# Performance work log

Hardware: AMD Instinct MI355X
Metric: run time of the kernel (lower is better)

## Reference

```python
import jax, jax.numpy as jnp
import numpy as np

L, H, NH, FF = 12, 768, 12, 3072
HD = H // NH
B, T = 8, 512
SCALE = 1.0 / float(np.sqrt(HD))
EPS = 1e-12


def setup_inputs() -> dict:
    key = jax.random.key(0)
    ks = jax.random.split(key, 10)
    s = jnp.float32(0.02)

    def p(k, shape):
        return jax.random.normal(k, shape, dtype=jnp.float32) * s

    return {
        "hidden_states": jax.random.normal(ks[0], (B, T, H), dtype=jnp.float32),
        "attention_mask": jnp.ones((B, T), dtype=jnp.float32),
        "Wq": p(ks[1], (L, H, H)), "bq": jnp.zeros((L, H), jnp.float32),
        "Wk": p(ks[2], (L, H, H)), "bk": jnp.zeros((L, H), jnp.float32),
        "Wv": p(ks[3], (L, H, H)), "bv": jnp.zeros((L, H), jnp.float32),
        "Wao": p(ks[4], (L, H, H)), "bao": jnp.zeros((L, H), jnp.float32),
        "ln1_g": jnp.ones((L, H), jnp.float32), "ln1_b": jnp.zeros((L, H), jnp.float32),
        "Wi": p(ks[5], (L, H, FF)), "bi": jnp.zeros((L, FF), jnp.float32),
        "Wo": p(ks[6], (L, FF, H)), "bo": jnp.zeros((L, H), jnp.float32),
        "ln2_g": jnp.ones((L, H), jnp.float32), "ln2_b": jnp.zeros((L, H), jnp.float32),
    }


def _layernorm(x, g, b):
    m = jnp.mean(x, axis=-1, keepdims=True)
    v = jnp.mean((x - m) ** 2, axis=-1, keepdims=True)
    return (x - m) * jax.lax.rsqrt(v + EPS) * g + b


def _encoder(hidden_states, attention_mask, params):
    # additive mask: (1 - mask) * -10000, broadcast to [B, 1, 1, T]
    add_mask = (1.0 - attention_mask)[:, None, None, :] * -10000.0

    def layer(x, p):
        wq, bq, wk, bk, wv, bv, wao, bao, g1, b1, wi, bi, wo, bo, g2, b2 = p
        q = (x @ wq + bq).reshape(B, T, NH, HD)
        k = (x @ wk + bk).reshape(B, T, NH, HD)
        v = (x @ wv + bv).reshape(B, T, NH, HD)
        scores = jnp.einsum('bihd,bjhd->bhij', q, k) * SCALE + add_mask
        probs = jax.nn.softmax(scores, axis=-1)  # dropout p=0 (eval)
        ctx = jnp.einsum('bhij,bjhd->bihd', probs, v).reshape(B, T, H)
        attn_out = _layernorm(ctx @ wao + bao + x, g1, b1)
        ff = jax.nn.gelu(attn_out @ wi + bi, approximate=False)
        out = _layernorm(ff @ wo + bo + attn_out, g2, b2)
        return out, None

    out, _ = jax.lax.scan(layer, hidden_states, params)
    return out


def reference(hidden_states, attention_mask, Wq, bq, Wk, bk, Wv, bv, Wao, bao,
              ln1_g, ln1_b, Wi, bi, Wo, bo, ln2_g, ln2_b):
    params = (Wq, bq, Wk, bk, Wv, bv, Wao, bao, ln1_g, ln1_b, Wi, bi, Wo, bo, ln2_g, ln2_b)
    return _encoder(hidden_states, attention_mask, params)
```

## Files before the change

kernel.cpp:

```cpp
#include <hip/hip_runtime.h>
#include <hip/hip_bf16.h>

typedef __bf16 bf16;
typedef __attribute__((ext_vector_type(8))) __bf16 bf16x8;
typedef __attribute__((ext_vector_type(4))) float f32x4;

#define MFMA16(a, b, c) __builtin_amdgcn_mfma_f32_16x16x32_bf16((a), (b), (c), 0, 0, 0)

#define WAIT_VM(N) asm volatile("s_waitcnt vmcnt(" #N ")" ::: "memory")
#define BAR() do { __builtin_amdgcn_s_barrier(); __builtin_amdgcn_sched_barrier(0); } while (0)
#define SYNC_VM(N) do { WAIT_VM(N); BAR(); } while (0)
#define SYNC_LGKM() do { asm volatile("s_waitcnt lgkmcnt(0)" ::: "memory"); BAR(); } while (0)

__device__ __forceinline__ void async16(const bf16* g, bf16* l) {
    __builtin_amdgcn_global_load_lds((__attribute__((address_space(1))) void*)(g),
                                     (__attribute__((address_space(3))) void*)(l), 16, 0, 0);
}

__device__ __forceinline__ void xcd_swizzle2(int& bx, int& by) {
    const int gx = gridDim.x, gy = gridDim.y;
    const int nwg = gx * gy;
    const int lin = blockIdx.x + gx * blockIdx.y;
    const int xcd = lin & 7, seq = lin >> 3;
    const int q = nwg >> 3, r = nwg & 7;
    const int nl = (xcd < r ? xcd * (q + 1) : r * (q + 1) + (xcd - r) * q) + seq;
    bx = nl % gx;
    by = nl / gx;
}
__device__ __forceinline__ void xcd_swizzle3(int& bx, int& by, int& bz) {
    const int gx = gridDim.x, gy = gridDim.y;
    const int nwg = gx * gy * gridDim.z;
    const int lin = blockIdx.x + gx * (blockIdx.y + gy * blockIdx.z);
    const int xcd = lin & 7, seq = lin >> 3;
    const int q = nwg >> 3, r = nwg & 7;
    const int nl = (xcd < r ? xcd * (q + 1) : r * (q + 1) + (xcd - r) * q) + seq;
    bx = nl % gx;
    const int t = nl / gx;
    by = t % gy;
    bz = t / gy;
}

__device__ __forceinline__ void xpose_tile(
    int id, const float* Wq, const float* Wk, const float* Wv, const float* Wao,
    const float* Wi, const float* Wo, bf16* wT, bf16* tile, int tid)
{
    const float* src; bf16* dst; int Nd;
    if (id < 576) {
        const int w = id / 144; id -= w * 144;
        Nd = 768;
        src = (w == 0) ? Wq : (w == 1) ? Wk : (w == 2) ? Wv : Wao;
        dst = wT + (size_t)w * 589824;
    } else if (id < 1152) {
        id -= 576; Nd = 3072; src = Wi; dst = wT + 2359296;
    } else {
        id -= 1152; Nd = 768; src = Wo; dst = wT + 4718592;
    }
    const int Kd = (Nd == 3072) ? 768 : ((src == Wo) ? 3072 : 768);
    const int tn = Nd >> 6;
    const int tr = id / tn, tc = id - tr * tn;
    const int r0 = tr * 64, c0 = tc * 64;

#pragma unroll
    for (int i = 0; i < 4; i++) {
        const int idx = i * 256 + tid;
        const int r = idx >> 4, c4 = (idx & 15) * 4;
        const float4 f = *(const float4*)(src + (size_t)(r0 + r) * Nd + c0 + c4);
        alignas(8) bf16 q[4] = {(bf16)f.x, (bf16)f.y, (bf16)f.z, (bf16)f.w};
        *(ushort4*)(tile + r * 68 + c4) = *(ushort4*)q;
    }
    __syncthreads();
#pragma unroll
    for (int i = 0; i < 4; i++) {
        const int idx = i * 256 + tid;
        const int n = idx >> 4, kc = (idx & 15) * 4;
        alignas(8) bf16 tmp[4];
#pragma unroll
        for (int e = 0; e < 4; e++) tmp[e] = tile[(kc + e) * 68 + n];
        *(ushort4*)(dst + (size_t)(c0 + n) * Kd + r0 + kc) = *(ushort4*)tmp;
    }
}

template <int MODE, int BM, int PACK>
__global__ __launch_bounds__(256) void gemm_kernel(
    const bf16* __restrict__ A, const bf16* __restrict__ WT,
    const float* __restrict__ b0, const float* __restrict__ b1, const float* __restrict__ b2,
    int s1, int s2,
    void* __restrict__ o0, void* __restrict__ o1, bf16* __restrict__ vTout,
    const float* __restrict__ xWq, const float* __restrict__ xWk,
    const float* __restrict__ xWv, const float* __restrict__ xWao,
    bf16* __restrict__ wTnext,
    int N, int K, int Kpart)
{
    constexpr int MT = BM / 32;
    constexpr int SBYTES = (2 * (BM * 32) + 2 * (128 * 32)) * 2;
    __shared__ __align__(16) char smem[SBYTES];
    bf16* sA = (bf16*)smem;
    bf16* sB = (bf16*)(smem + 2 * BM * 32 * 2);

    const int tid = threadIdx.x;

    if (PACK && blockIdx.z == 1) {
        const int flat = blockIdx.y * gridDim.x + blockIdx.x;
        if (flat < 576 && wTnext)
            xpose_tile(flat, xWq, xWk, xWv, xWao, nullptr, nullptr, wTnext,
                       (bf16*)smem, tid);
        return;
    }
    const int kslice = PACK ? 0 : blockIdx.z;

    const int lane = tid & 63;
    const int wave = tid >> 6;
    const int quad = lane >> 4;
    const int l15  = lane & 15;
    const int wm   = (wave >> 1) * (BM / 2);
    const int wn   = (wave & 1) * 64;

    int bxs, bys;
    xcd_swizzle2(bxs, bys);
    const int bm = bys * BM;
    const int bn = bxs * 128;
    const int kbase = kslice * Kpart;

    f32x4 acc[MT][4];
#pragma unroll
    for (int i = 0; i < MT; i++)
#pragma unroll
        for (int j = 0; j < 4; j++)
#pragma unroll
            for (int r = 0; r < 4; r++) acc[i][j][r] = 0.0f;

    const int idx1 = tid + 256;
    const int ra0 = tid >> 2,  ca0 = (((tid  & 3) ^ ((ra0 >> 1) & 3)) * 8);
    const int rb1 = idx1 >> 2, cb1 = (((idx1 & 3) ^ ((rb1 >> 1) & 3)) * 8);

    const bf16* Arow0 = A + (size_t)(bm + ra0) * K + kbase + ca0;
    const bf16* Arow1 = (BM == 128) ? A + (size_t)(bm + rb1) * K + kbase + cb1 : A;
    const bf16* Brow0 = WT + (size_t)(bn + ra0) * K + kbase + ca0;
    const bf16* Brow1 = WT + (size_t)(bn + rb1) * K + kbase + cb1;

    const int nk = Kpart >> 5;

    async16(Arow0, sA + tid * 8);
    if (BM == 128) async16(Arow1, sA + idx1 * 8);
    async16(Brow0, sB + tid * 8);
    async16(Brow1, sB + idx1 * 8);

    const int chF = (quad ^ ((l15 >> 1) & 3)) * 8;

    int cur = 0;
    for (int kt = 0; kt < nk; kt++) {
        if (kt + 1 < nk) {
            const int ko = (kt + 1) * 32;
            const int nb = (cur ^ 1);
            async16(Arow0 + ko, sA + nb * BM * 32 + tid * 8);
            if (BM == 128) async16(Arow1 + ko, sA + nb * BM * 32 + idx1 * 8);
            async16(Brow0 + ko, sB + nb * 128 * 32 + tid * 8);
            async16(Brow1 + ko, sB + nb * 128 * 32 + idx1 * 8);
            if (BM == 128) SYNC_VM(4);
            else           SYNC_VM(3);
        } else {
            SYNC_VM(0);
        }
        const bf16* sAc = sA + cur * BM * 32;
        const bf16* sBc = sB + cur * 128 * 32;
        bf16x8 af[MT], bfr[4];
#pragma unroll
        for (int i = 0; i < MT; i++)
            af[i] = *(const bf16x8*)(sAc + (wm + i * 16 + l15) * 32 + chF);
#pragma unroll
        for (int i = 0; i < 4; i++)
            bfr[i] = *(const bf16x8*)(sBc + (wn + i * 16 + l15) * 32 + chF);
#pragma unroll
        for (int mt = 0; mt < MT; mt++)
#pragma unroll
            for (int nt = 0; nt < 4; nt++)
                acc[mt][nt] = MFMA16(af[mt], bfr[nt], acc[mt][nt]);
        SYNC_LGKM();
        cur ^= 1;
    }

    void* outp = (kslice == 0) ? o0 : o1;

#pragma unroll
    for (int nt = 0; nt < 4; nt++) {
        const int col = bn + wn + nt * 16 + l15;
        float bias = 0.0f;
        if (MODE != 1)
            bias = (col < s1) ? b0[col] : (col < s2) ? b1[col - s1] : b2[col - s2];
        if (MODE == 0 && col >= s2) {
            const int hd = col - s2, h = hd >> 6, d = hd & 63;
#pragma unroll
            for (int mt = 0; mt < MT; mt++) {
                const int row0 = bm + wm + mt * 16 + quad * 4;
                const int b = row0 >> 9, key = row0 & 511;
                alignas(8) bf16 tmp[4];
#pragma unroll
                for (int r = 0; r < 4; r++) tmp[r] = (bf16)(acc[mt][nt][r] + bias);
                *(ushort4*)(vTout + (((size_t)(b * 12 + h)) << 15) + (d << 9) + key)
                    = *(ushort4*)tmp;
            }
        } else {
#pragma unroll
            for (int mt = 0; mt < MT; mt++) {
#pragma unroll
                for (int r = 0; r < 4; r++) {
                    const int row = bm + wm + mt * 16 + quad * 4 + r;
                    float v = acc[mt][nt][r] + bias;
                    if (MODE == 2) v = 0.5f * v * (1.0f + erff(v * 0.70710678118654752f));
                    if (MODE == 1)      ((float*)outp)[(size_t)row * N + col] = v;
                    else if (MODE == 0) ((bf16*)outp)[(size_t)row * s2 + col] = (bf16)v;
                    else                ((bf16*)outp)[(size_t)row * N + col] = (bf16)v;
                }
            }
        }
    }
}

__global__ __launch_bounds__(256) void attn_kernel(
    const bf16* __restrict__ qk, const bf16* __restrict__ vT,
    const float* __restrict__ mask, bf16* __restrict__ ctx)
{
    int bxs, bys, bzs;
    xcd_swizzle3(bxs, bys, bzs);
    const int b = bzs, h = bys, q0 = bxs * 32;
    const int bh = b * 12 + h;
    const int tid = threadIdx.x, lane = tid & 63, wave = tid >> 6;
    const int quad = lane >> 4, l15 = lane & 15;
    const int mt = wave & 1;
    const int whi = wave >> 1;

    __shared__ __align__(16) bf16 sKV[2][64 * 64];
    __shared__ __align__(16) bf16 sS[32 * 520];
    __shared__ float sAM[512];
    __shared__ float sRed[256];
    __shared__ float sRow[32];

    for (int i = tid; i < 512; i += 256)
        sAM[i] = (1.0f - mask[b * 512 + i]) * -10000.0f;

    const size_t RS = 1536;
    const bf16* Qrow = qk + (size_t)(b * 512 + q0 + mt * 16 + l15) * RS + h * 64;
    const bf16x8 aQ0 = *(const bf16x8*)(Qrow + quad * 8);
    const bf16x8 aQ1 = *(const bf16x8*)(Qrow + 32 + quad * 8);

    const int c0 = tid, c1 = tid + 256;
    const int r0 = c0 >> 3, r1 = c1 >> 3;
    const int sc0 = ((c0 & 7) ^ (r0 & 7)) * 8;
    const int sc1 = ((c1 & 7) ^ (r1 & 7)) * 8;

    const bf16* Kbase = qk + (size_t)(b * 512) * RS + 768 + h * 64;

    async16(Kbase + (size_t)(r0) * RS + sc0, (bf16*)sKV[0] + c0 * 8);
    async16(Kbase + (size_t)(r1) * RS + sc1, (bf16*)sKV[0] + c1 * 8);

#pragma unroll
    for (int kt = 0; kt < 8; kt++) {
        const int cur = kt & 1;
        if (kt < 7) {
            async16(Kbase + (size_t)((kt + 1) * 64 + r0) * RS + sc0, (bf16*)sKV[cur ^ 1] + c0 * 8);
            async16(Kbase + (size_t)((kt + 1) * 64 + r1) * RS + sc1, (bf16*)sKV[cur ^ 1] + c1 * 8);
            SYNC_VM(2);
        } else {
            SYNC_VM(0);
        }
#pragma unroll
        for (int n = 0; n < 2; n++) {
            const int nt = whi * 2 + n;
            const int krow = nt * 16 + l15;
            const int sw = krow & 7;
            bf16x8 bK0 = *(const bf16x8*)(sKV[cur] + krow * 64 + ((quad ^ sw) * 8));
            bf16x8 bK1 = *(const bf16x8*)(sKV[cur] + krow * 64 + (((4 + quad) ^ sw) * 8));
            f32x4 accS;
#pragma unroll
            for (int r = 0; r < 4; r++) accS[r] = 0.0f;
            accS = MFMA16(aQ0, bK0, accS);
            accS = MFMA16(aQ1, bK1, accS);
#pragma unroll
            for (int r = 0; r < 4; r++) {
                const int row = mt * 16 + quad * 4 + r;
                sS[row * 520 + kt * 64 + nt * 16 + l15] = (bf16)accS[r];
            }
        }
        SYNC_LGKM();
    }

    const bf16* Vbase = vT + (size_t)bh * 64 * 512;
    async16(Vbase + (size_t)r0 * 512 + sc0, (bf16*)sKV[0] + c0 * 8);
    async16(Vbase + (size_t)r1 * 512 + sc1, (bf16*)sKV[0] + c1 * 8);

    {
        const int r = tid >> 3, p = tid & 7;
        float mx = -1e30f;
#pragma unroll
        for (int t = 0; t < 8; t++) {
            const int v0 = (p + 8 * t) * 8;
            bf16x8 pv = *(const bf16x8*)(sS + r * 520 + v0);
#pragma unroll
            for (int e = 0; e < 8; e++)
                mx = fmaxf(mx, (float)pv[e] * 0.125f + sAM[v0 + e]);
        }
        sRed[r * 8 + p] = mx;
        SYNC_LGKM();
#pragma unroll
        for (int q = 0; q < 8; q++) mx = fmaxf(mx, sRed[r * 8 + q]);
        float sum = 0.0f;
#pragma unroll
        for (int t = 0; t < 8; t++) {
            const int v0 = (p + 8 * t) * 8;
            bf16x8 pv = *(const bf16x8*)(sS + r * 520 + v0);
            bf16x8 ev;
#pragma unroll
            for (int e = 0; e < 8; e++) {
                const float x = __expf((float)pv[e] * 0.125f + sAM[v0 + e] - mx);
                sum += x;
                ev[e] = (bf16)x;
            }
            *(bf16x8*)(sS + r * 520 + v0) = ev;
        }
        SYNC_LGKM();
        sRed[r * 8 + p] = sum;
        SYNC_LGKM();
        if (p == 0) {
            float s = 0.0f;
#pragma unroll
            for (int q = 0; q < 8; q++) s += sRed[r * 8 + q];
            sRow[r] = s;
        }
    }

    f32x4 accO[2];
#pragma unroll
    for (int i = 0; i < 2; i++)
#pragma unroll
        for (int r = 0; r < 4; r++) accO[i][r] = 0.0f;

#pragma unroll
    for (int kt = 0; kt < 8; kt++) {
        const int cur = kt & 1;
        if (kt < 7) {
            async16(Vbase + (size_t)r0 * 512 + (kt + 1) * 64 + sc0, (bf16*)sKV[cur ^ 1] + c0 * 8);
            async16(Vbase + (size_t)r1 * 512 + (kt + 1) * 64 + sc1, (bf16*)sKV[cur ^ 1] + c1 * 8);
            SYNC_VM(2);
        } else {
            SYNC_VM(0);
        }
#pragma unroll
        for (int kk = 0; kk < 2; kk++) {
            bf16x8 aP = *(const bf16x8*)(sS + (mt * 16 + l15) * 520 + kt * 64 + kk * 32 + quad * 8);
#pragma unroll
            for (int n = 0; n < 2; n++) {
                const int vrow = whi * 32 + n * 16 + l15;
                bf16x8 bV = *(const bf16x8*)(sKV[cur] + vrow * 64 + (((kk * 4 + quad) ^ (vrow & 7)) * 8));
                accO[n] = MFMA16(aP, bV, accO[n]);
            }
        }
        SYNC_LGKM();
    }
#pragma unroll
    for (int n = 0; n < 2; n++) {
#pragma unroll
        for (int r = 0; r < 4; r++) {
            const int row = mt * 16 + quad * 4 + r;
            const float o = accO[n][r] / sRow[row];
            ctx[(size_t)(b * 512 + q0 + row) * 768 + h * 64 + whi * 32 + n * 16 + l15] = (bf16)o;
        }
    }
}

template <int NP, int PACK>
__global__ __launch_bounds__(256) void ln_kernel(
    const float* p0, const float* p1,
    const float* bias, const float* resid,
    const float* g, const float* bb,
    bf16* out_bf, float* out_f32,
    const float* xWi, const float* xWo, bf16* wTnext)
{
    if constexpr (PACK) {
        __shared__ __align__(16) bf16 xtile[64 * 68];
        if (blockIdx.x >= 4096) {
            if (wTnext)
                xpose_tile(576 + (blockIdx.x - 4096), nullptr, nullptr, nullptr,
                           nullptr, xWi, xWo, wTnext, xtile, threadIdx.x);
            return;
        }
    }
    const int row = blockIdx.x;
    const int tid = threadIdx.x;
    __shared__ float sS[4], sQ[4];

    float x[3], s = 0.0f, sq = 0.0f;
#pragma unroll
    for (int j = 0; j < 3; j++) {
        const int c = tid + j * 256;
        const size_t idx = (size_t)row * 768 + c;
        float v = p0[idx] + bias[c] + resid[idx];
        if (NP > 1) v += p1[idx];
        x[j] = v; s += v; sq += v * v;
    }
#pragma unroll
    for (int off = 32; off; off >>= 1) { s += __shfl_down(s, off); sq += __shfl_down(sq, off); }
    if ((tid & 63) == 0) { sS[tid >> 6] = s; sQ[tid >> 6] = sq; }
    __syncthreads();
    s  = sS[0] + sS[1] + sS[2] + sS[3];
    sq = sQ[0] + sQ[1] + sQ[2] + sQ[3];
    const float mean = s * (1.0f / 768.0f);
    float var = sq * (1.0f / 768.0f) - mean * mean;
    var = fmaxf(var, 0.0f);
    const float rstd = rsqrtf(var + 1e-12f);
#pragma unroll
    for (int j = 0; j < 3; j++) {
        const int c = tid + j * 256;
        const float v = (x[j] - mean) * rstd * g[c] + bb[c];
        out_bf[(size_t)row * 768 + c] = (bf16)v;
        out_f32[(size_t)row * 768 + c] = v;
    }
}

__global__ __launch_bounds__(256) void prep_kernel(
    const float* __restrict__ hidden, bf16* __restrict__ xb,
    const float* __restrict__ Wq, const float* __restrict__ Wk,
    const float* __restrict__ Wv, const float* __restrict__ Wao,
    const float* __restrict__ Wi, const float* __restrict__ Wo,
    bf16* __restrict__ wT)
{
    __shared__ __align__(16) bf16 tile[64 * 68];
    if (blockIdx.x < 12288) {
        const int i = blockIdx.x * 256 + threadIdx.x;
        if (i < 3145728) xb[i] = (bf16)hidden[i];
        return;
    }
    xpose_tile(blockIdx.x - 12288, Wq, Wk, Wv, Wao, Wi, Wo, wT, tile, threadIdx.x);
}

extern "C" void kernel_launch(void* const* d_in, const int* in_sizes, int n_in,
                              void* d_out, int out_size, void* d_ws, size_t ws_size,
                              hipStream_t stream)
{
    const float* hidden = (const float*)d_in[0];
    const float* mask   = (const float*)d_in[1];
    const float* Wq  = (const float*)d_in[2];  const float* bq  = (const float*)d_in[3];
    const float* Wk  = (const float*)d_in[4];  const float* bk  = (const float*)d_in[5];
    const float* Wv  = (const float*)d_in[6];  const float* bv  = (const float*)d_in[7];
    const float* Wao = (const float*)d_in[8];  const float* bao = (const float*)d_in[9];
    const float* g1  = (const float*)d_in[10]; const float* be1 = (const float*)d_in[11];
    const float* Wi  = (const float*)d_in[12]; const float* bi  = (const float*)d_in[13];
    const float* Wo  = (const float*)d_in[14]; const float* bo  = (const float*)d_in[15];
    const float* g2  = (const float*)d_in[16]; const float* be2 = (const float*)d_in[17];

    char* ws = (char*)d_ws;
    bf16*  wT    = (bf16*)(ws);
    bf16*  qk    = (bf16*)(ws + 14155776);
    bf16*  vT    = (bf16*)(ws + 26738688);
    bf16*  ctx   = (bf16*)(ws + 33030144);
    bf16*  attnb = (bf16*)(ws + 39321600);
    bf16*  xb    = (bf16*)(ws + 45613056);
    float* xf    = (float*)(ws + 51904512);
    float* attnf = (float*)(ws + 64487424);
    bf16*  ffh   = (bf16*)(ws + 14155776);
    float* pA0   = (float*)(ws + 14155776);
    float* pA1   = (float*)(ws + 77070336);
    float* pF0   = (float*)(ws + 77070336);
    float* pF1   = (float*)(ws + 51904512);

    prep_kernel<<<14016, 256, 0, stream>>>(hidden, xb, Wq, Wk, Wv, Wao, Wi, Wo, wT);

    for (int l = 0; l < 12; l++) {
        const int ln = l + 1;
        bf16* wTn = (l < 11) ? wT : nullptr;

        gemm_kernel<0, 64, 0><<<dim3(18, 64, 1), 256, 0, stream>>>(
            xb, wT, bq + l * 768, bk + l * 768, bv + l * 768, 768, 1536,
            qk, nullptr, vT, nullptr, nullptr, nullptr, nullptr, nullptr,
            2304, 768, 768);

        attn_kernel<<<dim3(16, 12, 8), 256, 0, stream>>>(qk, vT, mask, ctx);

        gemm_kernel<1, 64, 0><<<dim3(6, 64, 2), 256, 0, stream>>>(
            ctx, wT + 1769472, nullptr, nullptr, nullptr, 0, 0,
            pA0, pA1, nullptr, nullptr, nullptr, nullptr, nullptr, nullptr,
            768, 768, 384);

        const float* resid1 = (l == 0) ? hidden : xf;
        ln_kernel<2, 0><<<4096, 256, 0, stream>>>(
            pA0, pA1, bao + l * 768, resid1, g1 + l * 768, be1 + l * 768,
            attnb, attnf, nullptr, nullptr, nullptr);

        gemm_kernel<2, 128, 1><<<dim3(24, 32, 2), 256, 0, stream>>>(
            attnb, wT + 2359296, bi + l * 3072, bi + l * 3072, bi + l * 3072, 3072, 3072,
            ffh, nullptr, nullptr,
            Wq + (size_t)(ln % 12) * 589824, Wk + (size_t)(ln % 12) * 589824,
            Wv + (size_t)(ln % 12) * 589824, Wao + (size_t)(ln % 12) * 589824, wTn,
            3072, 768, 768);

        gemm_kernel<1, 64, 0><<<dim3(6, 64, 2), 256, 0, stream>>>(
            ffh, wT + 4718592, nullptr, nullptr, nullptr, 0, 0,
            pF0, pF1, nullptr, nullptr, nullptr, nullptr, nullptr, nullptr,
            768, 3072, 1536);

        float* f32dst = (l == 11) ? (float*)d_out : xf;
        ln_kernel<2, 1><<<4096 + 1152, 256, 0, stream>>>(
            pF0, pF1, bo + l * 768, attnf, g2 + l * 768, be2 + l * 768,
            xb, f32dst,
            Wi + (size_t)(ln % 12) * 2359296, Wo + (size_t)(ln % 12) * 2359296, wTn);
    }
}
```

Before: 2.361 ms.

## Use BK=64 GEMM tiles and move QKV/Wao weight packing into LN1

The GEMM kernel now stages 64-wide K tiles with an 8-way XOR swizzle and issues two MFMAs per fragment pair per stage. This halves the number of barrier and wait iterations, at the cost of doubling LDS use per block. The BM=128 FFN-up variant is dropped in favour of BM=64 tiles over a 24x64 grid. The next layer's Wq/Wk/Wv/Wao transpose-pack moves out of the FFN-up GEMM launch into the first LayerNorm launch as extra blocks, removing the extra z-slice from the GEMM grid.

```diff
diff --git a/kernel.cpp b/kernel.cpp
--- a/kernel.cpp
+++ b/kernel.cpp
@@ -44,18 +44,17 @@
     int id, const float* Wq, const float* Wk, const float* Wv, const float* Wao,
     const float* Wi, const float* Wo, bf16* wT, bf16* tile, int tid)
 {
-    const float* src; bf16* dst; int Nd;
+    const float* src; bf16* dst; int Nd, Kd;
     if (id < 576) {
         const int w = id / 144; id -= w * 144;
-        Nd = 768;
+        Nd = 768; Kd = 768;
         src = (w == 0) ? Wq : (w == 1) ? Wk : (w == 2) ? Wv : Wao;
         dst = wT + (size_t)w * 589824;
     } else if (id < 1152) {
-        id -= 576; Nd = 3072; src = Wi; dst = wT + 2359296;
+        id -= 576; Nd = 3072; Kd = 768; src = Wi; dst = wT + 2359296;
     } else {
-        id -= 1152; Nd = 768; src = Wo; dst = wT + 4718592;
-    }
-    const int Kd = (Nd == 3072) ? 768 : ((src == Wo) ? 3072 : 768);
+        id -= 1152; Nd = 768; Kd = 3072; src = Wo; dst = wT + 4718592;
+    }
     const int tn = Nd >> 6;
     const int tr = id / tn, tc = id - tr * tn;
     const int r0 = tr * 64, c0 = tc * 64;
@@ -80,106 +79,103 @@
     }
 }
 
-template <int MODE, int BM, int PACK>
+template <int MODE>
 __global__ __launch_bounds__(256) void gemm_kernel(
     const bf16* __restrict__ A, const bf16* __restrict__ WT,
     const float* __restrict__ b0, const float* __restrict__ b1, const float* __restrict__ b2,
     int s1, int s2,
     void* __restrict__ o0, void* __restrict__ o1, bf16* __restrict__ vTout,
-    const float* __restrict__ xWq, const float* __restrict__ xWk,
-    const float* __restrict__ xWv, const float* __restrict__ xWao,
-    bf16* __restrict__ wTnext,
     int N, int K, int Kpart)
 {
-    constexpr int MT = BM / 32;
-    constexpr int SBYTES = (2 * (BM * 32) + 2 * (128 * 32)) * 2;
-    __shared__ __align__(16) char smem[SBYTES];
-    bf16* sA = (bf16*)smem;
-    bf16* sB = (bf16*)(smem + 2 * BM * 32 * 2);
-
-    const int tid = threadIdx.x;
-
-    if (PACK && blockIdx.z == 1) {
-        const int flat = blockIdx.y * gridDim.x + blockIdx.x;
-        if (flat < 576 && wTnext)
-            xpose_tile(flat, xWq, xWk, xWv, xWao, nullptr, nullptr, wTnext,
-                       (bf16*)smem, tid);
-        return;
-    }
-    const int kslice = PACK ? 0 : blockIdx.z;
-
+    __shared__ __align__(16) bf16 sA[2][64 * 64];
+    __shared__ __align__(16) bf16 sB[2][128 * 64];
+
+    const int tid  = threadIdx.x;
     const int lane = tid & 63;
     const int wave = tid >> 6;
     const int quad = lane >> 4;
     const int l15  = lane & 15;
-    const int wm   = (wave >> 1) * (BM / 2);
+    const int wm   = (wave >> 1) * 32;
     const int wn   = (wave & 1) * 64;
 
     int bxs, bys;
     xcd_swizzle2(bxs, bys);
-    const int bm = bys * BM;
+    const int bm = bys * 64;
     const int bn = bxs * 128;
-    const int kbase = kslice * Kpart;
-
-    f32x4 acc[MT][4];
-#pragma unroll
-    for (int i = 0; i < MT; i++)
+    const int kbase = blockIdx.z * Kpart;
+
+    f32x4 acc[2][4];
+#pragma unroll
+    for (int i = 0; i < 2; i++)
 #pragma unroll
         for (int j = 0; j < 4; j++)
 #pragma unroll
             for (int r = 0; r < 4; r++) acc[i][j][r] = 0.0f;
 
-    const int idx1 = tid + 256;
-    const int ra0 = tid >> 2,  ca0 = (((tid  & 3) ^ ((ra0 >> 1) & 3)) * 8);
-    const int rb1 = idx1 >> 2, cb1 = (((idx1 & 3) ^ ((rb1 >> 1) & 3)) * 8);
-
-    const bf16* Arow0 = A + (size_t)(bm + ra0) * K + kbase + ca0;
-    const bf16* Arow1 = (BM == 128) ? A + (size_t)(bm + rb1) * K + kbase + cb1 : A;
-    const bf16* Brow0 = WT + (size_t)(bn + ra0) * K + kbase + ca0;
-    const bf16* Brow1 = WT + (size_t)(bn + rb1) * K + kbase + cb1;
-
-    const int nk = Kpart >> 5;
-
-    async16(Arow0, sA + tid * 8);
-    if (BM == 128) async16(Arow1, sA + idx1 * 8);
-    async16(Brow0, sB + tid * 8);
-    async16(Brow1, sB + idx1 * 8);
-
-    const int chF = (quad ^ ((l15 >> 1) & 3)) * 8;
+    const int cA0 = tid,       cA1 = tid + 256;
+    const int cB0 = tid,       cB1 = tid + 256;
+    const int cB2 = tid + 512, cB3 = tid + 768;
+    const int rA0 = cA0 >> 3, kA0 = (((cA0 & 7) ^ (rA0 & 7)) * 8);
+    const int rA1 = cA1 >> 3, kA1 = (((cA1 & 7) ^ (rA1 & 7)) * 8);
+    const int rB0 = cB0 >> 3, kB0 = (((cB0 & 7) ^ (rB0 & 7)) * 8);
+    const int rB1 = cB1 >> 3, kB1 = (((cB1 & 7) ^ (rB1 & 7)) * 8);
+    const int rB2 = cB2 >> 3, kB2 = (((cB2 & 7) ^ (rB2 & 7)) * 8);
+    const int rB3 = cB3 >> 3, kB3 = (((cB3 & 7) ^ (rB3 & 7)) * 8);
+
+    const bf16* A0 = A  + (size_t)(bm + rA0) * K + kbase + kA0;
+    const bf16* A1 = A  + (size_t)(bm + rA1) * K + kbase + kA1;
+    const bf16* B0 = WT + (size_t)(bn + rB0) * K + kbase + kB0;
+    const bf16* B1 = WT + (size_t)(bn + rB1) * K + kbase + kB1;
+    const bf16* B2 = WT + (size_t)(bn + rB2) * K + kbase + kB2;
+    const bf16* B3 = WT + (size_t)(bn + rB3) * K + kbase + kB3;
+
+    const int nk = Kpart >> 6;
+
+    auto stage = [&](int kt, int buf) {
+        const int ko = kt * 64;
+        async16(A0 + ko, sA[buf] + cA0 * 8);
+        async16(A1 + ko, sA[buf] + cA1 * 8);
+        async16(B0 + ko, sB[buf] + cB0 * 8);
+        async16(B1 + ko, sB[buf] + cB1 * 8);
+        async16(B2 + ko, sB[buf] + cB2 * 8);
+        async16(B3 + ko, sB[buf] + cB3 * 8);
+    };
+
+    stage(0, 0);
+
+    const int xr = (l15 & 7);
 
     int cur = 0;
     for (int kt = 0; kt < nk; kt++) {
         if (kt + 1 < nk) {
-            const int ko = (kt + 1) * 32;
-            const int nb = (cur ^ 1);
-            async16(Arow0 + ko, sA + nb * BM * 32 + tid * 8);
-            if (BM == 128) async16(Arow1 + ko, sA + nb * BM * 32 + idx1 * 8);
-            async16(Brow0 + ko, sB + nb * 128 * 32 + tid * 8);
-            async16(Brow1 + ko, sB + nb * 128 * 32 + idx1 * 8);
-            if (BM == 128) SYNC_VM(4);
-            else           SYNC_VM(3);
+            stage(kt + 1, cur ^ 1);
+            SYNC_VM(6);
         } else {
             SYNC_VM(0);
         }
-        const bf16* sAc = sA + cur * BM * 32;
-        const bf16* sBc = sB + cur * 128 * 32;
-        bf16x8 af[MT], bfr[4];
-#pragma unroll
-        for (int i = 0; i < MT; i++)
-            af[i] = *(const bf16x8*)(sAc + (wm + i * 16 + l15) * 32 + chF);
-#pragma unroll
-        for (int i = 0; i < 4; i++)
-            bfr[i] = *(const bf16x8*)(sBc + (wn + i * 16 + l15) * 32 + chF);
-#pragma unroll
-        for (int mt = 0; mt < MT; mt++)
+        bf16x8 af[2][2], bfr[4][2];
+#pragma unroll
+        for (int kk = 0; kk < 2; kk++) {
+            const int ch = ((kk * 4 + quad) ^ xr) * 8;
+#pragma unroll
+            for (int i = 0; i < 2; i++)
+                af[i][kk] = *(const bf16x8*)(sA[cur] + (wm + i * 16 + l15) * 64 + ch);
+#pragma unroll
+            for (int i = 0; i < 4; i++)
+                bfr[i][kk] = *(const bf16x8*)(sB[cur] + (wn + i * 16 + l15) * 64 + ch);
+        }
+#pragma unroll
+        for (int mt = 0; mt < 2; mt++)
 #pragma unroll
             for (int nt = 0; nt < 4; nt++)
-                acc[mt][nt] = MFMA16(af[mt], bfr[nt], acc[mt][nt]);
+#pragma unroll
+                for (int kk = 0; kk < 2; kk++)
+                    acc[mt][nt] = MFMA16(af[mt][kk], bfr[nt][kk], acc[mt][nt]);
         SYNC_LGKM();
         cur ^= 1;
     }
 
-    void* outp = (kslice == 0) ? o0 : o1;
+    void* outp = (blockIdx.z == 0) ? o0 : o1;
 
 #pragma unroll
     for (int nt = 0; nt < 4; nt++) {
@@ -190,7 +186,7 @@
         if (MODE == 0 && col >= s2) {
             const int hd = col - s2, h = hd >> 6, d = hd & 63;
 #pragma unroll
-            for (int mt = 0; mt < MT; mt++) {
+            for (int mt = 0; mt < 2; mt++) {
                 const int row0 = bm + wm + mt * 16 + quad * 4;
                 const int b = row0 >> 9, key = row0 & 511;
                 alignas(8) bf16 tmp[4];
@@ -201,7 +197,7 @@
             }
         } else {
 #pragma unroll
-            for (int mt = 0; mt < MT; mt++) {
+            for (int mt = 0; mt < 2; mt++) {
 #pragma unroll
                 for (int r = 0; r < 4; r++) {
                     const int row = bm + wm + mt * 16 + quad * 4 + r;
@@ -367,20 +363,26 @@
     }
 }
 
-template <int NP, int PACK>
+template <int NP, int PACKSEL>
 __global__ __launch_bounds__(256) void ln_kernel(
     const float* p0, const float* p1,
     const float* bias, const float* resid,
     const float* g, const float* bb,
     bf16* out_bf, float* out_f32,
-    const float* xWi, const float* xWo, bf16* wTnext)
+    const float* xW0, const float* xW1, const float* xW2, const float* xW3,
+    bf16* wTnext)
 {
-    if constexpr (PACK) {
-        __shared__ __align__(16) bf16 xtile[64 * 68];
+    if constexpr (PACKSEL > 0) {
         if (blockIdx.x >= 4096) {
-            if (wTnext)
-                xpose_tile(576 + (blockIdx.x - 4096), nullptr, nullptr, nullptr,
-                           nullptr, xWi, xWo, wTnext, xtile, threadIdx.x);
+            __shared__ __align__(16) bf16 xtile[64 * 68];
+            if (wTnext) {
+                if (PACKSEL == 1)
+                    xpose_tile(blockIdx.x - 4096, xW0, xW1, xW2, xW3,
+                               nullptr, nullptr, wTnext, xtile, threadIdx.x);
+                else
+                    xpose_tile(576 + (blockIdx.x - 4096), nullptr, nullptr, nullptr,
+                               nullptr, xW0, xW1, wTnext, xtile, threadIdx.x);
+            }
             return;
         }
     }
@@ -465,42 +467,38 @@
     prep_kernel<<<14016, 256, 0, stream>>>(hidden, xb, Wq, Wk, Wv, Wao, Wi, Wo, wT);
 
     for (int l = 0; l < 12; l++) {
-        const int ln = l + 1;
+        const int ln = (l + 1) % 12;
         bf16* wTn = (l < 11) ? wT : nullptr;
 
-        gemm_kernel<0, 64, 0><<<dim3(18, 64, 1), 256, 0, stream>>>(
+        gemm_kernel<0><<<dim3(18, 64, 1), 256, 0, stream>>>(
             xb, wT, bq + l * 768, bk + l * 768, bv + l * 768, 768, 1536,
-            qk, nullptr, vT, nullptr, nullptr, nullptr, nullptr, nullptr,
-            2304, 768, 768);
+            qk, nullptr, vT, 2304, 768, 768);
 
         attn_kernel<<<dim3(16, 12, 8), 256, 0, stream>>>(qk, vT, mask, ctx);
 
-        gemm_kernel<1, 64, 0><<<dim3(6, 64, 2), 256, 0, stream>>>(
+        gemm_kernel<1><<<dim3(6, 64, 2), 256, 0, stream>>>(
             ctx, wT + 1769472, nullptr, nullptr, nullptr, 0, 0,
-            pA0, pA1, nullptr, nullptr, nullptr, nullptr, nullptr, nullptr,
-            768, 768, 384);
+            pA0, pA1, nullptr, 768, 768, 384);
 
         const float* resid1 = (l == 0) ? hidden : xf;
-        ln_kernel<2, 0><<<4096, 256, 0, stream>>>(
+        ln_kernel<2, 1><<<4096 + 576, 256, 0, stream>>>(
             pA0, pA1, bao + l * 768, resid1, g1 + l * 768, be1 + l * 768,
-            attnb, attnf, nullptr, nullptr, nullptr);
-
-        gemm_kernel<2, 128, 1><<<dim3(24, 32, 2), 256, 0, stream>>>(
+            attnb, attnf,
+            Wq + (size_t)ln * 589824, Wk + (size_t)ln * 589824,
+            Wv + (size_t)ln * 589824, Wao + (size_t)ln * 589824, wTn);
+
+        gemm_kernel<2><<<dim3(24, 64, 1), 256, 0, stream>>>(
             attnb, wT + 2359296, bi + l * 3072, bi + l * 3072, bi + l * 3072, 3072, 3072,
-            ffh, nullptr, nullptr,
-            Wq + (size_t)(ln % 12) * 589824, Wk + (size_t)(ln % 12) * 589824,
-            Wv + (size_t)(ln % 12) * 589824, Wao + (size_t)(ln % 12) * 589824, wTn,
-            3072, 768, 768);
-
-        gemm_kernel<1, 64, 0><<<dim3(6, 64, 2), 256, 0, stream>>>(
+            ffh, nullptr, nullptr, 3072, 768, 768);
+
+        gemm_kernel<1><<<dim3(6, 64, 2), 256, 0, stream>>>(
             ffh, wT + 4718592, nullptr, nullptr, nullptr, 0, 0,
-            pF0, pF1, nullptr, nullptr, nullptr, nullptr, nullptr, nullptr,
-            768, 3072, 1536);
+            pF0, pF1, nullptr, 768, 3072, 1536);
 
         float* f32dst = (l == 11) ? (float*)d_out : xf;
-        ln_kernel<2, 1><<<4096 + 1152, 256, 0, stream>>>(
+        ln_kernel<2, 2><<<4096 + 1152, 256, 0, stream>>>(
             pF0, pF1, bo + l * 768, attnf, g2 + l * 768, be2 + l * 768,
             xb, f32dst,
-            Wi + (size_t)(ln % 12) * 2359296, Wo + (size_t)(ln % 12) * 2359296, wTn);
-    }
-}
+            Wi + (size_t)ln * 2359296, Wo + (size_t)ln * 2359296, nullptr, nullptr, wTn);
+    }
+}
```

New measurement: 2.239 ms. 5.2% less time.
